# Performance work log

Measured on AMD Instinct MI355X. Metric: run time of the kernel, lower is better.

## Reference

```python
import jax, jax.numpy as jnp
import numpy as np

B, C, H, W, O, K = 4, 64, 128, 128, 64, 3


def setup_inputs() -> dict:
    key = jax.random.key(0)
    kx, ko, kw = jax.random.split(key, 3)
    x = jax.random.normal(kx, (B, C, H, W), dtype=jnp.float32)
    offset = jax.random.normal(ko, (B, 2 * K * K, H, W), dtype=jnp.float32)
    stdv = 1.0 / np.sqrt(C * K * K)
    weight = jax.random.uniform(kw, (O, C, K, K), dtype=jnp.float32,
                                minval=-stdv, maxval=stdv)
    return {"x": x, "offset": offset, "weight": weight}


def _deform_conv(x, offset, weight):
    b, c, h, w = x.shape
    o = weight.shape[0]
    k = weight.shape[2]
    kk = k * k
    # kernel tap displacements, flattened row-major (ki*K + kj), centered at 0
    taps = jnp.arange(k) - k // 2
    di = jnp.repeat(taps, k)            # [kk]
    dj = jnp.tile(taps, k)              # [kk]
    # base sampling coords: base_i[h,1,kk], base_j[1,w,kk]
    base_i = (jnp.arange(h)[:, None, None] + di).astype(jnp.float32)
    base_j = (jnp.arange(w)[None, :, None] + dj).astype(jnp.float32)
    # offset: [b, kk, 2, h, w] -> [b, h, w, kk, 2]
    off = offset.reshape(b, kk, 2, h, w).transpose(0, 3, 4, 1, 2)
    ci = off[..., 0] + base_i           # [b,h,w,kk] float sample row coords
    cj = off[..., 1] + base_j           # [b,h,w,kk] float sample col coords

    i_lt = jnp.floor(ci).astype(jnp.int32)
    i_rb = jnp.ceil(ci).astype(jnp.int32)
    j_lt = jnp.floor(cj).astype(jnp.int32)
    j_rb = jnp.ceil(cj).astype(jnp.int32)

    def gather(ii, jj):
        # out-of-bounds samples contribute 0 (matching the torch masking)
        inb = (ii >= 0) & (ii < h) & (jj >= 0) & (jj < w)
        ic = jnp.clip(ii, 0, h - 1)
        jc = jnp.clip(jj, 0, w - 1)
        # per-image gather: xb[:, i, j] with i,j of shape [h,w,kk] -> [c,h,w,kk]
        v = jax.vmap(lambda xb, i, j: xb[:, i, j])(x, ic, jc)  # [b,c,h,w,kk]
        return v * inb[:, None].astype(x.dtype)

    vals_lt = gather(i_lt, j_lt)
    vals_rb = gather(i_rb, j_rb)
    vals_rt = gather(i_lt, j_rb)
    vals_lb = gather(i_rb, j_lt)

    # fractional parts (gradient flows to offset only through these)
    fi = (ci - i_lt.astype(ci.dtype))[:, None]   # [b,1,h,w,kk]
    fj = (cj - j_lt.astype(cj.dtype))[:, None]

    vals_t = vals_lt + fj * (vals_rt - vals_lt)
    vals_b = vals_lb + fj * (vals_rb - vals_lb)
    mapped = vals_t + fi * (vals_b - vals_t)     # [b,c,h,w,kk]

    # final GEMM: weight [o, c*kk] x im2col-like [c*kk, b*h*w]
    return jnp.einsum('ock,bchwk->bohw', weight.reshape(o, c, kk), mapped)


def reference(x, offset, weight):
    return _deform_conv(x, offset, weight)
```

## Files before the change

kernel.cpp:

```cpp
#include <hip/hip_runtime.h>

namespace {
constexpr int B = 4, C = 64, H = 128, W = 128, O = 64, KK = 9;
constexpr int PREPT = 256;
constexpr int MAINT = 512;
constexpr int WF_ELEMS = KK * 2 * 4 * 64 * 8;
constexpr size_t XT_BYTES = (size_t)B * H * W * C * 2;
constexpr size_t WF_BYTES = (size_t)WF_ELEMS * 2;
constexpr size_t WS_NEED  = XT_BYTES + WF_BYTES;
}

typedef float    f32x4 __attribute__((ext_vector_type(4)));
typedef _Float16 f16x2 __attribute__((ext_vector_type(2)));
typedef _Float16 f16x8 __attribute__((ext_vector_type(8)));

__device__ __forceinline__ unsigned hpack2(float a, float b) {
  f16x2 v; v[0] = (_Float16)a; v[1] = (_Float16)b;
  return __builtin_bit_cast(unsigned, v);
}
__device__ __forceinline__ void gload16(const void* g, void* l) {
  __builtin_amdgcn_global_load_lds(
      (const __attribute__((address_space(1))) unsigned*)g,
      (__attribute__((address_space(3))) unsigned*)l, 16, 0, 0);
}

__global__ __launch_bounds__(PREPT)
void prep_fused(const float* __restrict__ x, const float* __restrict__ wgt,
                unsigned* __restrict__ xt_u32, unsigned short* __restrict__ wf) {
  __shared__ float st[64][65];
  const int t = threadIdx.x;

  const int gid = blockIdx.x * PREPT + t;
  if (gid < WF_ELEMS) {
    const int e = gid & 7, lane = (gid >> 3) & 63, mt = (gid >> 9) & 3;
    const int ks = (gid >> 11) & 1, tap = gid >> 12;
    const int o = mt * 16 + (lane & 15);
    const int c = ks * 32 + ((lane >> 4) << 3) + e;
    const _Float16 hv = (_Float16)wgt[(size_t)o * (C * KK) + c * KK + tap];
    wf[gid] = __builtin_bit_cast(unsigned short, hv);
  }

  const int half = blockIdx.x & 1, h = (blockIdx.x >> 1) & 127, b = blockIdx.x >> 8;
  const int w0 = half * 64;
#pragma unroll
  for (int it = 0; it < 16; ++it) {
    const int w = t & 63, c = it * 4 + (t >> 6);
    st[w][c] = x[((size_t)(b * C + c) * H + h) * W + w0 + w];
  }
  __syncthreads();
#pragma unroll
  for (int it = 0; it < 8; ++it) {
    const int idx = it * PREPT + t;
    const int w = idx >> 5, c2 = (idx & 31) * 2;
    xt_u32[(size_t)(((b * H + h) * W) + w0 + w) * 32 + (c2 >> 1)] = hpack2(st[w][c2], st[w][c2 + 1]);
  }
}

__global__ __launch_bounds__(MAINT) __attribute__((amdgpu_waves_per_eu(4)))
void deform_mfma(const float* __restrict__ offs, const char* __restrict__ xt,
                 const char* __restrict__ wfg, float* __restrict__ out) {
  __shared__ unsigned short s_wf[2][4096];
  __shared__ unsigned short s_m[128 * 64];
  __shared__ unsigned s_pw[8][KK][16][2];
  __shared__ unsigned s_pa[8][KK][16][4];

  const int t = threadIdx.x, l = t & 63, wid = t >> 6;
  const int nid = (blockIdx.x & 7) * 64 + (blockIdx.x >> 3);
  const int h = nid & 127, b = nid >> 7;
  const int wbase = wid * 16;

#pragma unroll
  for (int it = 0; it < 3; ++it) {
    const int item = it * 64 + l;
    if (item < KK * 16) {
      const int tap = item >> 4, pix = item & 15;
      const int ki = tap / 3, kj = tap - ki * 3;
      const int w = wbase + pix;
      const float* ob = offs + ((size_t)b * (2 * KK) + 2 * tap) * (H * W) + h * W + w;
      const float oi = ob[0], oj = ob[H * W];
      const float ci = oi + (float)(h + ki - 1);
      const float cj = oj + (float)(w + kj - 1);
      const float fli = floorf(ci), flj = floorf(cj);
      const int i0 = (int)fli, j0 = (int)flj, i1 = i0 + 1, j1 = j0 + 1;
      const float fi = ci - fli, fj = cj - flj, gi = 1.f - fi, gj = 1.f - fj;
      const bool bi0 = (unsigned)i0 < (unsigned)H, bi1 = (unsigned)i1 < (unsigned)H;
      const bool bj0 = (unsigned)j0 < (unsigned)W, bj1 = (unsigned)j1 < (unsigned)W;
      const int ic0 = min(max(i0, 0), H - 1), ic1 = min(max(i1, 0), H - 1);
      const int jc0 = min(max(j0, 0), W - 1), jc1 = min(max(j1, 0), W - 1);
      const float w00 = gi * gj * (float)(bi0 && bj0);
      const float w01 = gi * fj * (float)(bi0 && bj1);
      const float w10 = fi * gj * (float)(bi1 && bj0);
      const float w11 = fi * fj * (float)(bi1 && bj1);
      s_pw[wid][tap][pix][0] = hpack2(w00, w01);
      s_pw[wid][tap][pix][1] = hpack2(w10, w11);
      s_pa[wid][tap][pix][0] = (unsigned)(((b * H + ic0) * W + jc0) << 7);
      s_pa[wid][tap][pix][1] = (unsigned)(((b * H + ic0) * W + jc1) << 7);
      s_pa[wid][tap][pix][2] = (unsigned)(((b * H + ic1) * W + jc0) << 7);
      s_pa[wid][tap][pix][3] = (unsigned)(((b * H + ic1) * W + jc1) << 7);
    }
  }

  const int pix8 = l >> 3, oct = l & 7, cb = oct << 4;

  char* smb = (char*)s_m;
  const int wb  = ((wid * 16 + pix8) << 7) + ((oct ^ pix8) << 4);
  const int rr  = wid * 16 + (l & 15);
  const int rd0 = (rr << 7) + ((((l >> 4)    ) ^ (l & 7)) << 4);
  const int rd1 = (rr << 7) + (((4 + (l >> 4)) ^ (l & 7)) << 4);

  f32x4 acc[4];
#pragma unroll
  for (int mt = 0; mt < 4; ++mt) acc[mt] = (f32x4)0.f;

  uint4 g[2][4];
#define ISSUE(TAPX, HS) do {                                                   \
    const uint4 ad = *(const uint4*)&s_pa[wid][(TAPX)][(HS) * 8 + pix8][0];    \
    g[HS][0] = *(const uint4*)(xt + ad.x + cb);                                \
    g[HS][1] = *(const uint4*)(xt + ad.y + cb);                                \
    g[HS][2] = *(const uint4*)(xt + ad.z + cb);                                \
    g[HS][3] = *(const uint4*)(xt + ad.w + cb);                                \
  } while (0)

#define LERPH(c0_, c1_, c2_, c3_) __builtin_bit_cast(unsigned, (f16x2)(        \
    __builtin_bit_cast(f16x2, c0_) * W00 + __builtin_bit_cast(f16x2, c1_) * W01 + \
    __builtin_bit_cast(f16x2, c2_) * W10 + __builtin_bit_cast(f16x2, c3_) * W11))

#define STAGE(TAPV, HS) do {                                                   \
    const uint2 pk = *(const uint2*)&s_pw[wid][(TAPV)][(HS) * 8 + pix8][0];    \
    const f16x2 pa_ = __builtin_bit_cast(f16x2, pk.x);                         \
    const f16x2 pb_ = __builtin_bit_cast(f16x2, pk.y);                         \
    const f16x2 W00 = {pa_[0], pa_[0]}, W01 = {pa_[1], pa_[1]};                \
    const f16x2 W10 = {pb_[0], pb_[0]}, W11 = {pb_[1], pb_[1]};                \
    uint4* gc = g[HS];                                                         \
    uint4 r;                                                                   \
    r.x = LERPH(gc[0].x, gc[1].x, gc[2].x, gc[3].x);                           \
    r.y = LERPH(gc[0].y, gc[1].y, gc[2].y, gc[3].y);                           \
    r.z = LERPH(gc[0].z, gc[1].z, gc[2].z, gc[3].z);                           \
    r.w = LERPH(gc[0].w, gc[1].w, gc[2].w, gc[3].w);                           \
    *(uint4*)(smb + wb + (HS) * 1024) = r;                                     \
  } while (0)

  gload16(wfg + (size_t)t * 16, (char*)s_wf + t * 16);
  ISSUE(0, 0);
  ISSUE(0, 1);

#pragma unroll 1
  for (int tap = 0; tap < KK; ++tap) {
    __syncthreads();

    if (tap + 1 < KK) {
      gload16(wfg + (size_t)(tap + 1) * 8192 + t * 16,
              (char*)s_wf + ((tap + 1) & 1) * 8192 + t * 16);
    }

    STAGE(tap, 0);
    if (tap + 1 < KK) ISSUE(tap + 1, 0);
    STAGE(tap, 1);
    if (tap + 1 < KK) ISSUE(tap + 1, 1);

    const char* wl = (const char*)s_wf + (tap & 1) * 8192;
    const f16x8 b0 = *(const f16x8*)(smb + rd0);
    const f16x8 b1 = *(const f16x8*)(smb + rd1);
#pragma unroll
    for (int mt = 0; mt < 4; ++mt) {
      const f16x8 a0 = *(const f16x8*)(wl + mt * 1024 + l * 16);
      acc[mt] = __builtin_amdgcn_mfma_f32_16x16x32_f16(a0, b0, acc[mt], 0, 0, 0);
    }
#pragma unroll
    for (int mt = 0; mt < 4; ++mt) {
      const f16x8 a1 = *(const f16x8*)(wl + 4096 + mt * 1024 + l * 16);
      acc[mt] = __builtin_amdgcn_mfma_f32_16x16x32_f16(a1, b1, acc[mt], 0, 0, 0);
    }
  }
#undef ISSUE
#undef LERPH
#undef STAGE

#pragma unroll
  for (int mt = 0; mt < 4; ++mt)
#pragma unroll
    for (int j = 0; j < 4; ++j) {
      const int o = mt * 16 + ((l >> 4) << 2) + j;
      out[((size_t)(b * O + o) * H + h) * W + wbase + (l & 15)] = acc[mt][j];
    }
}

namespace fb {
constexpr int WT = 32, CH = 16, NCHUNK = 4, KC = 144, WPAD = 68;
}
__global__ __launch_bounds__(PREPT, 2)
void deform_conv_fused(const float* __restrict__ x, const float* __restrict__ offs,
                       const float* __restrict__ wgt, float* __restrict__ out) {
  using namespace fb;
  __shared__ int   s_i0[KK][WT];
  __shared__ int   s_j0[KK][WT];
  __shared__ float s_fi[KK][WT];
  __shared__ float s_fj[KK][WT];
  __shared__ float s_w[KC][WPAD];
  __shared__ float s_m[KC][WT + 1];
  const int t = threadIdx.x;
  const int nwt = W / WT;
  const int wt = blockIdx.x % nwt, h = (blockIdx.x / nwt) % H, b = blockIdx.x / (nwt * H);
  const int w0 = wt * WT;
  for (int idx = t; idx < KK * WT; idx += PREPT) {
    const int k = idx / WT, p = idx % WT, w = w0 + p;
    const float oi = offs[(((size_t)b * (2 * KK) + 2 * k) * H + h) * W + w];
    const float oj = offs[(((size_t)b * (2 * KK) + 2 * k + 1) * H + h) * W + w];
    const float ci = oi + (float)(h + (k / 3) - 1), cj = oj + (float)(w + (k % 3) - 1);
    const float fli = floorf(ci), flj = floorf(cj);
    s_i0[k][p] = (int)fli; s_j0[k][p] = (int)flj;
    s_fi[k][p] = ci - fli; s_fj[k][p] = cj - flj;
  }
  float acc[8];
#pragma unroll
  for (int i = 0; i < 8; ++i) acc[i] = 0.f;
  const int p = t & (WT - 1), ob = (t >> 5) * 8;
  for (int cc = 0; cc < NCHUNK; ++cc) {
    const int c0 = cc * CH;
    __syncthreads();
    for (int idx = t; idx < O * KC; idx += PREPT)
      s_w[idx % KC][idx / KC] = wgt[(size_t)(idx / KC) * (C * KK) + (size_t)c0 * KK + idx % KC];
    for (int idx = t; idx < CH * KK * WT; idx += PREPT) {
      const int pp = idx & (WT - 1), rest = idx >> 5, k = rest % KK, cl = rest / KK;
      const int i0 = s_i0[k][pp], j0 = s_j0[k][pp], i1 = i0 + 1, j1 = j0 + 1;
      const float fi = s_fi[k][pp], fj = s_fj[k][pp];
      const float* xb = x + (size_t)(b * C + c0 + cl) * H * W;
      const float v00 = ((unsigned)i0 < (unsigned)H && (unsigned)j0 < (unsigned)W) ? xb[i0 * W + j0] : 0.f;
      const float v01 = ((unsigned)i0 < (unsigned)H && (unsigned)j1 < (unsigned)W) ? xb[i0 * W + j1] : 0.f;
      const float v10 = ((unsigned)i1 < (unsigned)H && (unsigned)j0 < (unsigned)W) ? xb[i1 * W + j0] : 0.f;
      const float v11 = ((unsigned)i1 < (unsigned)H && (unsigned)j1 < (unsigned)W) ? xb[i1 * W + j1] : 0.f;
      const float top = v00 + fj * (v01 - v00), bot = v10 + fj * (v11 - v10);
      s_m[cl * KK + k][pp] = top + fi * (bot - top);
    }
    __syncthreads();
#pragma unroll 4
    for (int k = 0; k < KC; ++k) {
      const float a = s_m[k][p];
      const float4 wv0 = *reinterpret_cast<const float4*>(&s_w[k][ob]);
      const float4 wv1 = *reinterpret_cast<const float4*>(&s_w[k][ob + 4]);
      acc[0] += a * wv0.x; acc[1] += a * wv0.y; acc[2] += a * wv0.z; acc[3] += a * wv0.w;
      acc[4] += a * wv1.x; acc[5] += a * wv1.y; acc[6] += a * wv1.z; acc[7] += a * wv1.w;
    }
  }
#pragma unroll
  for (int i = 0; i < 8; ++i)
    out[(((size_t)b * O + ob + i) * H + h) * W + w0 + p] = acc[i];
}

extern "C" void kernel_launch(void* const* d_in, const int* in_sizes, int n_in,
                              void* d_out, int out_size, void* d_ws, size_t ws_size,
                              hipStream_t stream) {
  const float* x    = (const float*)d_in[0];
  const float* offs = (const float*)d_in[1];
  const float* wgt  = (const float*)d_in[2];
  float* out = (float*)d_out;

  if (ws_size < WS_NEED) {
    deform_conv_fused<<<B * H * (W / 32), PREPT, 0, stream>>>(x, offs, wgt, out);
    return;
  }
  char* xt = (char*)d_ws;
  unsigned short* wf = (unsigned short*)(xt + XT_BYTES);

  prep_fused<<<B * H * 2, PREPT, 0, stream>>>(x, wgt, (unsigned*)xt, wf);
  deform_mfma<<<B * H, MAINT, 0, stream>>>(offs, xt, (const char*)wf, out);
}
```

Baseline: 30.31 us.

## Pack sample coords into one word, vectorize prep loads, raise waves, set MFMA priority

The four precomputed gather addresses per tap and pixel are replaced by a single packed 32-bit word holding the clamped row and column indices. Each thread unpacks these indices when it issues its gathers, which cuts LDS footprint and LDS read traffic. The prep kernel now reads x with float4 loads instead of scalar loads. The occupancy hint goes from 4 to 6 waves per EU, and s_setprio wraps the MFMA section. The higher wave target could force register spilling.

```diff
diff --git a/kernel.cpp b/kernel.cpp
--- a/kernel.cpp
+++ b/kernel.cpp
@@ -43,9 +43,11 @@
   const int half = blockIdx.x & 1, h = (blockIdx.x >> 1) & 127, b = blockIdx.x >> 8;
   const int w0 = half * 64;
 #pragma unroll
-  for (int it = 0; it < 16; ++it) {
-    const int w = t & 63, c = it * 4 + (t >> 6);
-    st[w][c] = x[((size_t)(b * C + c) * H + h) * W + w0 + w];
+  for (int it = 0; it < 4; ++it) {
+    const int w4 = (t & 15) * 4, c = it * 16 + (t >> 4);
+    const float4 v = *(const float4*)&x[((size_t)(b * C + c) * H + h) * W + w0 + w4];
+    st[w4 + 0][c] = v.x; st[w4 + 1][c] = v.y;
+    st[w4 + 2][c] = v.z; st[w4 + 3][c] = v.w;
   }
   __syncthreads();
 #pragma unroll
@@ -56,13 +58,13 @@
   }
 }
 
-__global__ __launch_bounds__(MAINT) __attribute__((amdgpu_waves_per_eu(4)))
+__global__ __launch_bounds__(MAINT) __attribute__((amdgpu_waves_per_eu(6)))
 void deform_mfma(const float* __restrict__ offs, const char* __restrict__ xt,
                  const char* __restrict__ wfg, float* __restrict__ out) {
   __shared__ unsigned short s_wf[2][4096];
   __shared__ unsigned short s_m[128 * 64];
   __shared__ unsigned s_pw[8][KK][16][2];
-  __shared__ unsigned s_pa[8][KK][16][4];
+  __shared__ unsigned s_pp[8][KK][16];
 
   const int t = threadIdx.x, l = t & 63, wid = t >> 6;
   const int nid = (blockIdx.x & 7) * 64 + (blockIdx.x >> 3);
@@ -93,16 +95,16 @@
       const float w11 = fi * fj * (float)(bi1 && bj1);
       s_pw[wid][tap][pix][0] = hpack2(w00, w01);
       s_pw[wid][tap][pix][1] = hpack2(w10, w11);
-      s_pa[wid][tap][pix][0] = (unsigned)(((b * H + ic0) * W + jc0) << 7);
-      s_pa[wid][tap][pix][1] = (unsigned)(((b * H + ic0) * W + jc1) << 7);
-      s_pa[wid][tap][pix][2] = (unsigned)(((b * H + ic1) * W + jc0) << 7);
-      s_pa[wid][tap][pix][3] = (unsigned)(((b * H + ic1) * W + jc1) << 7);
+      s_pp[wid][tap][pix] = (unsigned)jc0 | ((unsigned)ic0 << 7) |
+                            ((unsigned)jc1 << 14) | ((unsigned)ic1 << 21);
     }
   }
 
   const int pix8 = l >> 3, oct = l & 7, cb = oct << 4;
+  const char* xb = xt + ((size_t)b * H * W << 7) + cb;
 
   char* smb = (char*)s_m;
+  char* smw = (char*)s_wf;
   const int wb  = ((wid * 16 + pix8) << 7) + ((oct ^ pix8) << 4);
   const int rr  = wid * 16 + (l & 15);
   const int rd0 = (rr << 7) + ((((l >> 4)    ) ^ (l & 7)) << 4);
@@ -114,11 +116,15 @@
 
   uint4 g[2][4];
 #define ISSUE(TAPX, HS) do {                                                   \
-    const uint4 ad = *(const uint4*)&s_pa[wid][(TAPX)][(HS) * 8 + pix8][0];    \
-    g[HS][0] = *(const uint4*)(xt + ad.x + cb);                                \
-    g[HS][1] = *(const uint4*)(xt + ad.y + cb);                                \
-    g[HS][2] = *(const uint4*)(xt + ad.z + cb);                                \
-    g[HS][3] = *(const uint4*)(xt + ad.w + cb);                                \
+    const unsigned v_ = s_pp[wid][(TAPX)][(HS) * 8 + pix8];                    \
+    const unsigned i0s = v_ & 0x3F80u;                                         \
+    const unsigned j0_ = v_ & 0x7Fu;                                           \
+    const unsigned j1_ = (v_ >> 14) & 0x7Fu;                                   \
+    const unsigned i1s = (v_ >> 14) & 0x3F80u;                                 \
+    g[HS][0] = *(const uint4*)(xb + ((size_t)(i0s | j0_) << 7));               \
+    g[HS][1] = *(const uint4*)(xb + ((size_t)(i0s | j1_) << 7));               \
+    g[HS][2] = *(const uint4*)(xb + ((size_t)(i1s | j0_) << 7));               \
+    g[HS][3] = *(const uint4*)(xb + ((size_t)(i1s | j1_) << 7));               \
   } while (0)
 
 #define LERPH(c0_, c1_, c2_, c3_) __builtin_bit_cast(unsigned, (f16x2)(        \
@@ -140,7 +146,7 @@
     *(uint4*)(smb + wb + (HS) * 1024) = r;                                     \
   } while (0)
 
-  gload16(wfg + (size_t)t * 16, (char*)s_wf + t * 16);
+  gload16(wfg + (size_t)t * 16, smw + t * 16);
   ISSUE(0, 0);
   ISSUE(0, 1);
 
@@ -148,19 +154,19 @@
   for (int tap = 0; tap < KK; ++tap) {
     __syncthreads();
 
-    if (tap + 1 < KK) {
+    if (tap + 1 < KK)
       gload16(wfg + (size_t)(tap + 1) * 8192 + t * 16,
-              (char*)s_wf + ((tap + 1) & 1) * 8192 + t * 16);
-    }
+              smw + ((tap + 1) & 1) * 8192 + t * 16);
 
     STAGE(tap, 0);
     if (tap + 1 < KK) ISSUE(tap + 1, 0);
     STAGE(tap, 1);
     if (tap + 1 < KK) ISSUE(tap + 1, 1);
 
-    const char* wl = (const char*)s_wf + (tap & 1) * 8192;
+    const char* wl = smw + (tap & 1) * 8192;
     const f16x8 b0 = *(const f16x8*)(smb + rd0);
     const f16x8 b1 = *(const f16x8*)(smb + rd1);
+    __builtin_amdgcn_s_setprio(1);
 #pragma unroll
     for (int mt = 0; mt < 4; ++mt) {
       const f16x8 a0 = *(const f16x8*)(wl + mt * 1024 + l * 16);
@@ -171,6 +177,7 @@
       const f16x8 a1 = *(const f16x8*)(wl + 4096 + mt * 1024 + l * 16);
       acc[mt] = __builtin_amdgcn_mfma_f32_16x16x32_f16(a1, b1, acc[mt], 0, 0, 0);
     }
+    __builtin_amdgcn_s_setprio(0);
   }
 #undef ISSUE
 #undef LERPH
```

Result: no change. 30.38 us (+0.2%).
